# Kernel tuning notes

Measured on AMD Instinct MI355X. Metric: run time of the kernel, lower is better.

## Reference

```python
import jax, jax.numpy as jnp
import numpy as np

ROI = 7   # roi_size
SR = 2    # sampling_ratio


def _interp_axis(t, size):
    # torchvision bilinear_interpolate semantics along one axis
    valid = (t > -1.0) & (t < size)
    t = jnp.clip(t, 0.0, None)
    low = jnp.minimum(jnp.floor(t).astype(jnp.int32), size - 1)
    high = jnp.minimum(low + 1, size - 1)
    t = jnp.where(low >= size - 1, low.astype(t.dtype), t)
    frac = t - low.astype(t.dtype)
    return valid, low, high, frac


def roi_align(fmap, boxes):
    """torchvision RoIAlign(output=(7,7), spatial_scale=1.0, sampling_ratio=2, aligned=False).
    fmap: [B,H,W,C] (channel-last; equivalent to torch's NCHW math), boxes: [N,5].
    Returns [N,C,ROI,ROI]."""
    B, H, W, C = fmap.shape
    N = boxes.shape[0]
    b = boxes[:, 0].astype(jnp.int32)
    x1, y1, x2, y2 = boxes[:, 1], boxes[:, 2], boxes[:, 3], boxes[:, 4]
    roi_w = jnp.maximum(x2 - x1, 1.0)
    roi_h = jnp.maximum(y2 - y1, 1.0)
    bin_w = roi_w / ROI
    bin_h = roi_h / ROI
    # per-bin sample offsets in bin units: (ph + (i+0.5)/SR) flattened over (bin, sample)
    grid = ((jnp.arange(ROI, dtype=fmap.dtype)[:, None] * SR
             + jnp.arange(SR, dtype=fmap.dtype)[None, :] + 0.5) / SR).reshape(-1)  # [ROI*SR]
    ys = y1[:, None] + grid[None, :] * bin_h[:, None]  # [N, S]
    xs = x1[:, None] + grid[None, :] * bin_w[:, None]  # [N, S]

    vy, yl, yh, ly = _interp_axis(ys, H)
    vx, xl, xh, lx = _interp_axis(xs, W)
    hy, hx = 1.0 - ly, 1.0 - lx

    bN = b[:, None, None]
    gather = lambda yi, xi: fmap[bN, yi[:, :, None], xi[:, None, :]]        # [N,S,S,C]
    wgt = lambda a, c: (a[:, :, None] * c[:, None, :])[..., None]           # [N,S,S,1]
    val = (wgt(hy, hx) * gather(yl, xl) + wgt(hy, lx) * gather(yl, xh)
           + wgt(ly, hx) * gather(yh, xl) + wgt(ly, lx) * gather(yh, xh))
    val = val * (vy[:, :, None] & vx[:, None, :])[..., None].astype(val.dtype)
    pooled = val.reshape(N, ROI, SR, ROI, SR, C).mean(axis=(2, 4))          # [N,ROI,ROI,C]
    return pooled.transpose(0, 3, 1, 2)                                     # [N,C,ROI,ROI]


def setup_inputs() -> dict:
    key = jax.random.key(0)
    kf, kb, kx1, kx2, ky1, ky2, kw1, kw2 = jax.random.split(key, 8)
    B, H, W, C = 8, 64, 64, 768
    N = 256
    feature_map = jax.random.normal(kf, (B, H, W, C), dtype=jnp.float32)
    bidx = jax.random.randint(kb, (N,), 0, B).astype(jnp.float32)
    x1 = jax.random.uniform(kx1, (N,)) * (W / 2)
    y1 = jax.random.uniform(ky1, (N,)) * (H / 2)
    x2 = x1 + 1.0 + jax.random.uniform(kx2, (N,)) * (W / 2 - 1.0)
    y2 = y1 + 1.0 + jax.random.uniform(ky2, (N,)) * (H / 2 - 1.0)
    lesion_bboxes = jnp.stack([bidx, x1, y1, x2, y2], axis=1).astype(jnp.float32)
    in_dim = C * ROI * ROI  # 37632
    W1 = jax.random.normal(kw1, (in_dim, 1024), dtype=jnp.float32) * 0.02
    b1 = jnp.zeros((1024,), dtype=jnp.float32)
    W2 = jax.random.normal(kw2, (1024, 512), dtype=jnp.float32) * 0.02
    b2 = jnp.zeros((512,), dtype=jnp.float32)
    return {"feature_map": feature_map, "lesion_bboxes": lesion_bboxes,
            "W1": W1, "b1": b1, "W2": W2, "b2": b2}


def reference(feature_map, lesion_bboxes, W1, b1, W2, b2):
    roi = roi_align(feature_map, lesion_bboxes)          # [N,C,7,7]
    flat = roi.reshape(roi.shape[0], -1)                  # channel-major flatten, as torch
    h = jax.nn.relu(flat @ W1 + b1)                       # Dropout(0.1) is identity in eval
    return h @ W2 + b2                                    # [N,512]
```

## Files before the change

### kernel.cpp

```cpp
#include <hip/hip_runtime.h>
#include <hip/hip_bf16.h>

typedef __attribute__((ext_vector_type(8))) short bfrag8;
typedef __attribute__((ext_vector_type(4))) float f32x4;

__device__ __forceinline__ unsigned short f2bf(float f) {
  unsigned int u = __float_as_uint(f);
  u += 0x7FFFu + ((u >> 16) & 1u);
  return (unsigned short)(u >> 16);
}

__device__ __forceinline__ void interp1(float t, int size, int& lo, int& hi, float& frac, bool& valid) {
  valid = (t > -1.0f) && (t < (float)size);
  t = fmaxf(t, 0.0f);
  lo = (int)t;
  if (lo > size - 1) lo = size - 1;
  hi = lo + 1; if (hi > size - 1) hi = size - 1;
  if (lo >= size - 1) t = (float)lo;
  frac = t - (float)lo;
}

__global__ __launch_bounds__(192) void roi_kernel(const float* __restrict__ fmap,
                                                  const float* __restrict__ boxes,
                                                  unsigned short* __restrict__ A) {
  const int bid = blockIdx.x;
  const int n = bid >> 2, q = bid & 3;
  const int t = threadIdx.x;
  __shared__ unsigned short T[192 * 49];

  const float* bx = boxes + n * 5;
  const int b = (int)bx[0];
  const float x1 = bx[1], y1 = bx[2], x2 = bx[3], y2 = bx[4];
  const float bw = fmaxf(x2 - x1, 1.0f) * (1.0f / 7.0f);
  const float bh = fmaxf(y2 - y1, 1.0f) * (1.0f / 7.0f);

  const int c = q * 192 + t;
  const float* fb = fmap + (size_t)b * 64 * 64 * 768 + c;

  for (int ph = 0; ph < 7; ph++) {
    int yl[2], yh[2]; float ly[2], hy[2]; bool vy[2];
    #pragma unroll
    for (int sy = 0; sy < 2; sy++) {
      float y = y1 + (ph * 2 + sy + 0.5f) * 0.5f * bh;
      interp1(y, 64, yl[sy], yh[sy], ly[sy], vy[sy]);
      hy[sy] = 1.0f - ly[sy];
    }
    float acc[7];
    #pragma unroll
    for (int pw = 0; pw < 7; pw++) acc[pw] = 0.0f;

    #pragma unroll
    for (int pw = 0; pw < 7; pw++) {
      #pragma unroll
      for (int sx = 0; sx < 2; sx++) {
        float x = x1 + (pw * 2 + sx + 0.5f) * 0.5f * bw;
        int xl, xh; float lx; bool vx;
        interp1(x, 64, xl, xh, lx, vx);
        float hx = 1.0f - lx;
        if (vx) {
          #pragma unroll
          for (int sy = 0; sy < 2; sy++) {
            if (vy[sy]) {
              float v00 = fb[(yl[sy] * 64 + xl) * 768];
              float v01 = fb[(yl[sy] * 64 + xh) * 768];
              float v10 = fb[(yh[sy] * 64 + xl) * 768];
              float v11 = fb[(yh[sy] * 64 + xh) * 768];
              acc[pw] += hy[sy] * (hx * v00 + lx * v01) + ly[sy] * (hx * v10 + lx * v11);
            }
          }
        }
      }
      T[t * 49 + ph * 7 + pw] = f2bf(acc[pw] * 0.25f);
    }
  }
  __syncthreads();
  const unsigned* Ts = (const unsigned*)T;
  unsigned* out = (unsigned*)(A + (size_t)n * 37632 + q * 9408);
  #pragma unroll 4
  for (int i = t; i < 4704; i += 192) out[i] = Ts[i];
}

template<int KT, int NT, int STEPS, int NNT>
__global__ __launch_bounds__(256, 2) void gemm_splitk(const unsigned short* __restrict__ A,
                                                      const float* __restrict__ B,
                                                      float* __restrict__ part) {
  __shared__ unsigned short Al[2][256 * 64];
  __shared__ unsigned short Bl[2][64 * 64];

  const int nwg = gridDim.x;
  const int bid = blockIdx.x;
  const int work = (bid & 7) * (nwg >> 3) + (bid >> 3);
  const int ks = work / NNT;
  const int nt = work - ks * NNT;
  const int n0 = nt * 64;
  const int k0 = ks * (STEPS * 64);

  const int t = (int)threadIdx.x;
  const int lane = t & 63, wid = t >> 6;

  f32x4 acc[4][4];
  #pragma unroll
  for (int i = 0; i < 4; i++)
    #pragma unroll
    for (int j = 0; j < 4; j++) acc[i][j] = (f32x4){0.f, 0.f, 0.f, 0.f};

  float4 b00, b01, b10, b11;

  auto issueA = [&](int buf, int s) {
    #pragma unroll
    for (int i = 0; i < 8; i++) {
      const int r0 = wid * 64 + i * 8;
      const int row = r0 + (lane >> 3);
      const int j = (lane & 7) ^ (row & 7);
      const unsigned short* g = A + (size_t)row * KT + (k0 + s * 64 + j * 8);
      __builtin_amdgcn_global_load_lds(
          (const __attribute__((address_space(1))) void*)g,
          (__attribute__((address_space(3))) void*)&Al[buf][r0 * 64],
          16, 0, 0);
    }
  };

  auto loadB = [&](int s) {
    const float* p = B + (size_t)(k0 + s * 64 + (t >> 4) * 2) * NT + n0 + (t & 15) * 4;
    b00 = *(const float4*)p;
    b01 = *(const float4*)(p + NT);
    b10 = *(const float4*)(p + 32 * (size_t)NT);
    b11 = *(const float4*)(p + 33 * (size_t)NT);
  };

  auto writeB = [&](int buf) {
    char* base = (char*)&Bl[buf][0];
    const int lo = ((t >> 4) & 3) * 4;
    const int nb = (t & 15) * 4;
    #define WRB(g, j, fa, fb_) { \
      int nn = nb + j; \
      int slot = (g) * 4 + wid; \
      unsigned v = (unsigned)f2bf(fa) | ((unsigned)f2bf(fb_) << 16); \
      *(unsigned*)(base + nn * 128 + ((slot ^ ((nn >> 3) & 7)) << 4) + lo) = v; }
    WRB(0, 0, b00.x, b01.x) WRB(0, 1, b00.y, b01.y)
    WRB(0, 2, b00.z, b01.z) WRB(0, 3, b00.w, b01.w)
    WRB(1, 0, b10.x, b11.x) WRB(1, 1, b10.y, b11.y)
    WRB(1, 2, b10.z, b11.z) WRB(1, 3, b10.w, b11.w)
    #undef WRB
  };

  auto compute = [&](int buf) {
    const char* abase = (const char*)&Al[buf][0];
    const char* bbase = (const char*)&Bl[buf][0];
    #pragma unroll
    for (int kk = 0; kk < 2; kk++) {
      const int slot = kk * 4 + (lane >> 4);
      bfrag8 af[4], bf[4];
      #pragma unroll
      for (int fm = 0; fm < 4; fm++) {
        const int r = wid * 64 + fm * 16 + (lane & 15);
        af[fm] = *(const bfrag8*)(abase + r * 128 + ((slot ^ (r & 7)) << 4));
      }
      #pragma unroll
      for (int fn = 0; fn < 4; fn++) {
        const int r = fn * 16 + (lane & 15);
        bf[fn] = *(const bfrag8*)(bbase + r * 128 + ((slot ^ ((r >> 3) & 7)) << 4));
      }
      #pragma unroll
      for (int fm = 0; fm < 4; fm++)
        #pragma unroll
        for (int fn = 0; fn < 4; fn++)
          acc[fm][fn] = __builtin_amdgcn_mfma_f32_16x16x32_bf16(af[fm], bf[fn], acc[fm][fn], 0, 0, 0);
    }
  };

  issueA(0, 0);
  loadB(0);
  writeB(0);
  __syncthreads();

  int buf = 0;
  for (int s = 0; s < STEPS; s++) {
    if (s + 1 < STEPS) {
      issueA(buf ^ 1, s + 1);
      loadB(s + 1);
    }
    compute(buf);
    if (s + 1 < STEPS) writeB(buf ^ 1);
    __syncthreads();
    buf ^= 1;
  }

  const int r4 = (lane >> 4) * 4, cn = lane & 15;
  #pragma unroll
  for (int fm = 0; fm < 4; fm++)
    #pragma unroll
    for (int fn = 0; fn < 4; fn++)
      #pragma unroll
      for (int q = 0; q < 4; q++) {
        int m = wid * 64 + fm * 16 + r4 + q;
        part[((size_t)ks * 256 + m) * NT + n0 + fn * 16 + cn] = acc[fm][fn][q];
      }
}

__global__ __launch_bounds__(256) void reduce_relu_28(const float* __restrict__ part,
                                                      const float* __restrict__ b1,
                                                      unsigned short* __restrict__ h) {
  const int i4 = blockIdx.x * 256 + threadIdx.x;
  const float4* p4 = (const float4*)part;
  float4 s = p4[i4];
  #pragma unroll
  for (int p = 1; p < 28; p++) {
    float4 v = p4[(size_t)p * 65536 + i4];
    s.x += v.x; s.y += v.y; s.z += v.z; s.w += v.w;
  }
  float4 bb = ((const float4*)b1)[i4 & 255];
  s.x = fmaxf(s.x + bb.x, 0.f); s.y = fmaxf(s.y + bb.y, 0.f);
  s.z = fmaxf(s.z + bb.z, 0.f); s.w = fmaxf(s.w + bb.w, 0.f);
  uint2 pk;
  pk.x = (unsigned)f2bf(s.x) | ((unsigned)f2bf(s.y) << 16);
  pk.y = (unsigned)f2bf(s.z) | ((unsigned)f2bf(s.w) << 16);
  ((uint2*)h)[i4] = pk;
}

__global__ __launch_bounds__(256) void reduce_bias_8(const float* __restrict__ part,
                                                     const float* __restrict__ b2,
                                                     float* __restrict__ out) {
  const int i4 = blockIdx.x * 256 + threadIdx.x;
  const float4* p4 = (const float4*)part;
  float4 s = p4[i4];
  #pragma unroll
  for (int p = 1; p < 8; p++) {
    float4 v = p4[(size_t)p * 32768 + i4];
    s.x += v.x; s.y += v.y; s.z += v.z; s.w += v.w;
  }
  float4 bb = ((const float4*)b2)[i4 & 127];
  s.x += bb.x; s.y += bb.y; s.z += bb.z; s.w += bb.w;
  ((float4*)out)[i4] = s;
}

extern "C" void kernel_launch(void* const* d_in, const int* in_sizes, int n_in,
                              void* d_out, int out_size, void* d_ws, size_t ws_size,
                              hipStream_t stream) {
  const float* fmap  = (const float*)d_in[0];
  const float* boxes = (const float*)d_in[1];
  const float* W1    = (const float*)d_in[2];
  const float* b1    = (const float*)d_in[3];
  const float* W2    = (const float*)d_in[4];
  const float* b2    = (const float*)d_in[5];
  float* out = (float*)d_out;

  char* ws = (char*)d_ws;
  unsigned short* Aroi = (unsigned short*)ws;
  float* part1 = (float*)(ws + 19267584);
  unsigned short* h = (unsigned short*)(ws + 19267584 + 29360128);
  float* part2 = (float*)(ws + 19267584 + 29360128 + 524288);

  roi_kernel<<<1024, 192, 0, stream>>>(fmap, boxes, Aroi);
  gemm_splitk<37632, 1024, 21, 16><<<448, 256, 0, stream>>>(Aroi, W1, part1);
  reduce_relu_28<<<256, 256, 0, stream>>>(part1, b1, h);
  gemm_splitk<1024, 512, 2, 8><<<64, 256, 0, stream>>>(h, W2, part2);
  reduce_bias_8<<<128, 256, 0, stream>>>(part2, b2, out);
}
```

Measured before the change: 399.2 us.

## Vectorize ROI gather with float4 channels and spread bins across threads

The RoI-align kernel now has each thread handle four consecutive channels using float4 loads, and distributes the 49 output bins across 8 thread groups in a 384-thread block. Before, each thread owned one channel and looped over all bins. The aim is fewer, wider global loads and more parallelism per block. The cost is more LDS bank traffic from the strided bf16 stores, and the final copy to global memory is widened to uint2.

```diff
diff --git a/kernel.cpp b/kernel.cpp
--- a/kernel.cpp
+++ b/kernel.cpp
@@ -20,12 +20,14 @@
   frac = t - (float)lo;
 }
 
-__global__ __launch_bounds__(192) void roi_kernel(const float* __restrict__ fmap,
+__global__ __launch_bounds__(384) void roi_kernel(const float* __restrict__ fmap,
                                                   const float* __restrict__ boxes,
                                                   unsigned short* __restrict__ A) {
   const int bid = blockIdx.x;
   const int n = bid >> 2, q = bid & 3;
   const int t = threadIdx.x;
+  const int cg = t % 48;
+  const int u  = t / 48;
   __shared__ unsigned short T[192 * 49];
 
   const float* bx = boxes + n * 5;
@@ -34,50 +36,50 @@
   const float bw = fmaxf(x2 - x1, 1.0f) * (1.0f / 7.0f);
   const float bh = fmaxf(y2 - y1, 1.0f) * (1.0f / 7.0f);
 
-  const int c = q * 192 + t;
+  const int c = q * 192 + cg * 4;
   const float* fb = fmap + (size_t)b * 64 * 64 * 768 + c;
 
-  for (int ph = 0; ph < 7; ph++) {
-    int yl[2], yh[2]; float ly[2], hy[2]; bool vy[2];
+  for (int bin = u; bin < 49; bin += 8) {
+    const int ph = bin / 7;
+    const int pw = bin - ph * 7;
+    float a0 = 0.f, a1 = 0.f, a2 = 0.f, a3 = 0.f;
     #pragma unroll
     for (int sy = 0; sy < 2; sy++) {
-      float y = y1 + (ph * 2 + sy + 0.5f) * 0.5f * bh;
-      interp1(y, 64, yl[sy], yh[sy], ly[sy], vy[sy]);
-      hy[sy] = 1.0f - ly[sy];
-    }
-    float acc[7];
-    #pragma unroll
-    for (int pw = 0; pw < 7; pw++) acc[pw] = 0.0f;
-
-    #pragma unroll
-    for (int pw = 0; pw < 7; pw++) {
+      float yv = y1 + (ph * 2 + sy + 0.5f) * 0.5f * bh;
+      int yl, yh; float fy; bool vy;
+      interp1(yv, 64, yl, yh, fy, vy);
+      const float gy = 1.0f - fy;
       #pragma unroll
       for (int sx = 0; sx < 2; sx++) {
-        float x = x1 + (pw * 2 + sx + 0.5f) * 0.5f * bw;
-        int xl, xh; float lx; bool vx;
-        interp1(x, 64, xl, xh, lx, vx);
-        float hx = 1.0f - lx;
-        if (vx) {
-          #pragma unroll
-          for (int sy = 0; sy < 2; sy++) {
-            if (vy[sy]) {
-              float v00 = fb[(yl[sy] * 64 + xl) * 768];
-              float v01 = fb[(yl[sy] * 64 + xh) * 768];
-              float v10 = fb[(yh[sy] * 64 + xl) * 768];
-              float v11 = fb[(yh[sy] * 64 + xh) * 768];
-              acc[pw] += hy[sy] * (hx * v00 + lx * v01) + ly[sy] * (hx * v10 + lx * v11);
-            }
-          }
+        float xv = x1 + (pw * 2 + sx + 0.5f) * 0.5f * bw;
+        int xl, xh; float fx; bool vx;
+        interp1(xv, 64, xl, xh, fx, vx);
+        if (vy && vx) {
+          const float gx = 1.0f - fx;
+          const float w00 = gy * gx, w01 = gy * fx, w10 = fy * gx, w11 = fy * fx;
+          const float* r0 = fb + (size_t)(yl * 64) * 768;
+          const float* r1 = fb + (size_t)(yh * 64) * 768;
+          float4 v00 = *(const float4*)(r0 + (size_t)xl * 768);
+          float4 v01 = *(const float4*)(r0 + (size_t)xh * 768);
+          float4 v10 = *(const float4*)(r1 + (size_t)xl * 768);
+          float4 v11 = *(const float4*)(r1 + (size_t)xh * 768);
+          a0 += w00 * v00.x + w01 * v01.x + w10 * v10.x + w11 * v11.x;
+          a1 += w00 * v00.y + w01 * v01.y + w10 * v10.y + w11 * v11.y;
+          a2 += w00 * v00.z + w01 * v01.z + w10 * v10.z + w11 * v11.z;
+          a3 += w00 * v00.w + w01 * v01.w + w10 * v10.w + w11 * v11.w;
         }
       }
-      T[t * 49 + ph * 7 + pw] = f2bf(acc[pw] * 0.25f);
-    }
+    }
+    const int base = cg * 196 + bin;
+    T[base]       = f2bf(a0 * 0.25f);
+    T[base + 49]  = f2bf(a1 * 0.25f);
+    T[base + 98]  = f2bf(a2 * 0.25f);
+    T[base + 147] = f2bf(a3 * 0.25f);
   }
   __syncthreads();
-  const unsigned* Ts = (const unsigned*)T;
-  unsigned* out = (unsigned*)(A + (size_t)n * 37632 + q * 9408);
-  #pragma unroll 4
-  for (int i = t; i < 4704; i += 192) out[i] = Ts[i];
+  const uint2* Ts = (const uint2*)T;
+  uint2* outp = (uint2*)(A + (size_t)n * 37632 + q * 9408);
+  for (int i = t; i < 2352; i += 384) outp[i] = Ts[i];
 }
 
 template<int KT, int NT, int STEPS, int NNT>
@@ -251,7 +253,7 @@
   unsigned short* h = (unsigned short*)(ws + 19267584 + 29360128);
   float* part2 = (float*)(ws + 19267584 + 29360128 + 524288);
 
-  roi_kernel<<<1024, 192, 0, stream>>>(fmap, boxes, Aroi);
+  roi_kernel<<<1024, 384, 0, stream>>>(fmap, boxes, Aroi);
   gemm_splitk<37632, 1024, 21, 16><<<448, 256, 0, stream>>>(Aroi, W1, part1);
   reduce_relu_28<<<256, 256, 0, stream>>>(part1, b1, h);
   gemm_splitk<1024, 512, 2, 8><<<64, 256, 0, stream>>>(h, W2, part2);
```

Result: faster. 340.8 us (-14.6%).
